# Kernel optimization log

Hardware: AMD Instinct MI355X
Metric: run time of the kernel (lower is better)

The kernel has to match this reference:

```python
import jax, jax.numpy as jnp
import numpy as np

N_NODES = 100000
N_EDGES = 1600000
N_CLASS = 26
HIDDEN = 128


def gcn_conv(x, W, b, row, col, ew, n):
    """PyG GCNConv with normalize=True, add_self_loops=True (fill 1.0).

    row/col/ew already include self-loops. x: [N, Fin], W: [Fin, Fout].
    """
    deg = jax.ops.segment_sum(ew, col, num_segments=n)            # [N]
    dis = jnp.where(deg > 0, jax.lax.rsqrt(jnp.maximum(deg, 1e-30)), 0.0)
    norm = dis[row] * ew * dis[col]                               # [E+N]
    h = x @ W                                                     # [N, Fout]
    msg = h[row] * norm[:, None]                                  # gather + scale
    out = jax.ops.segment_sum(msg, col, num_segments=n)           # scatter-add
    return out + b


def setup_inputs() -> dict:
    key = jax.random.key(0)
    k1, k2, k3, k4, k5, k6, k7, k8, k9 = jax.random.split(key, 9)
    x = jax.random.normal(k1, (N_NODES, N_CLASS), dtype=jnp.float32)
    edge_index = jax.random.randint(k2, (2, N_EDGES), 0, N_NODES, dtype=jnp.int64)
    edge_weight = jax.random.uniform(k3, (N_EDGES,), dtype=jnp.float32)
    s1 = 1.0 / np.sqrt(N_CLASS)
    s2 = 1.0 / np.sqrt(HIDDEN)
    W1 = jax.random.uniform(k4, (N_CLASS, HIDDEN), jnp.float32, -s1, s1)
    b1 = jnp.zeros((HIDDEN,), jnp.float32)
    W2 = jax.random.uniform(k5, (HIDDEN, HIDDEN), jnp.float32, -s2, s2)
    b2 = jnp.zeros((HIDDEN,), jnp.float32)
    Wfc = jax.random.uniform(k6, (HIDDEN, N_CLASS), jnp.float32, -s2, s2)
    bfc = jax.random.uniform(k7, (N_CLASS,), jnp.float32, -s2, s2)
    return {"x": x, "edge_index": edge_index, "edge_weight": edge_weight,
            "W1": W1, "b1": b1, "W2": W2, "b2": b2, "Wfc": Wfc, "bfc": bfc}


def reference(x, edge_index, edge_weight, W1, b1, W2, b2, Wfc, bfc):
    n = x.shape[0]
    loop = jnp.arange(n, dtype=edge_index.dtype)
    row = jnp.concatenate([edge_index[0], loop])   # sources (with self-loops)
    col = jnp.concatenate([edge_index[1], loop])   # targets
    ew = jnp.concatenate([edge_weight, jnp.ones((n,), edge_weight.dtype)])
    h = jax.nn.relu(gcn_conv(x, W1, b1, row, col, ew, n))
    h = jax.nn.relu(gcn_conv(h, W2, b2, row, col, ew, n))
    return h @ Wfc + bfc
```

## Files before the change

kernel.cpp:

```cpp
#include <hip/hip_runtime.h>
#include <hip/hip_fp16.h>

#define N_NODES 100000
#define N_EDGES 1600000
#define HIDDEN  128
#define N_CLASS 26

#define BUK_SHIFT 8
#define BUK_DSTS  256
#define NBUK      391
#define BUK_CAP   5120
#define PB_EDGES  4096
#define PB_BLOCKS ((N_EDGES + PB_EDGES - 1) / PB_EDGES)

typedef _Float16 f16x2 __attribute__((ext_vector_type(2)));

__device__ __forceinline__ float fdot2(__half2 a, __half2 b, float c) {
#if __has_builtin(__builtin_amdgcn_fdot2)
    union { __half2 h; f16x2 v; } ua, ub;
    ua.h = a; ub.h = b;
    return __builtin_amdgcn_fdot2(ua.v, ub.v, c, false);
#else
    float2 fa = __half22float2(a), fb = __half22float2(b);
    return c + fa.x * fb.x + fa.y * fb.y;
#endif
}

union U4 { uint4 u; __half2 h[4]; };
union U2 { uint2 u; __half2 h[2]; };
union UW { int i; __half2 h; };


__global__ __launch_bounds__(512) void bucket_kernel(const int* __restrict__ row,
                                                     const int* __restrict__ col,
                                                     const float* __restrict__ ew,
                                                     int* __restrict__ bukcnt,
                                                     int2* __restrict__ stage) {
    __shared__ int2 outst[PB_EDGES];
    __shared__ unsigned short bukof[PB_EDGES];
    __shared__ int cnt[NBUK], ofs[NBUK], cur[NBUK], gt[NBUK];
    __shared__ int sc[512];
    const int tid = threadIdx.x;
    const int e0 = blockIdx.x * PB_EDGES;
    const int nvalid = min(PB_EDGES, N_EDGES - e0);

    for (int b = tid; b < NBUK; b += 512) { cnt[b] = 0; cur[b] = 0; }
    __syncthreads();

    int mykey[8]; float myw[8]; int mybuk[8];
#pragma unroll
    for (int i = 0; i < 8; ++i) {
        int idx = tid + i * 512;
        mybuk[i] = -1;
        if (idx < nvalid) {
            int e = e0 + idx;
            int d = col[e], r = row[e];
            int buk = d >> BUK_SHIFT;
            mykey[i] = ((d & (BUK_DSTS - 1)) << 17) | r;
            myw[i] = ew[e];
            mybuk[i] = buk;
            atomicAdd(&cnt[buk], 1);
        }
    }
    __syncthreads();

    {
        int c = (tid < NBUK) ? cnt[tid] : 0;
        sc[tid] = c;
        __syncthreads();
        for (int o = 1; o < 512; o <<= 1) {
            int v = (tid >= o) ? sc[tid - o] : 0;
            __syncthreads();
            sc[tid] += v;
            __syncthreads();
        }
        if (tid < NBUK) ofs[tid] = sc[tid] - c;
        __syncthreads();
    }

#pragma unroll
    for (int i = 0; i < 8; ++i) {
        if (mybuk[i] >= 0) {
            int s = ofs[mybuk[i]] + atomicAdd(&cur[mybuk[i]], 1);
            outst[s] = make_int2(mykey[i], __float_as_int(myw[i]));
            bukof[s] = (unsigned short)mybuk[i];
        }
    }
    __syncthreads();

    if (tid < NBUK) {
        int c = cnt[tid];
        int gb = (c > 0) ? atomicAdd(&bukcnt[tid], c) : 0;
        gt[tid] = tid * BUK_CAP + gb;
    }
    __syncthreads();

    for (int i = tid; i < nvalid; i += 512) {
        int b = bukof[i];
        stage[(size_t)gt[b] + (i - ofs[b])] = outst[i];
    }
}


__global__ void bukscan_kernel(const int* __restrict__ bukcnt, int* __restrict__ bukbase,
                               int* __restrict__ start) {
    __shared__ int s[512];
    int tid = threadIdx.x;
    int c = (tid < NBUK) ? bukcnt[tid] : 0;
    s[tid] = c;
    __syncthreads();
    for (int o = 1; o < 512; o <<= 1) {
        int v = (tid >= o) ? s[tid - o] : 0;
        __syncthreads();
        s[tid] += v;
        __syncthreads();
    }
    if (tid < NBUK) bukbase[tid] = s[tid] - c;
    if (tid == 0) start[N_NODES] = N_EDGES;
}


__global__ __launch_bounds__(1024) void csr_kernel(const int2* __restrict__ stage,
                                                   const int* __restrict__ bukcnt,
                                                   const int* __restrict__ bukbase,
                                                   const float* __restrict__ x,
                                                   int* __restrict__ start,
                                                   float* __restrict__ dinv,
                                                   __half* __restrict__ x16,
                                                   int2* __restrict__ packed,
                                                   int* __restrict__ perm) {
    __shared__ unsigned int cnt5[BUK_DSTS];
    __shared__ int ofs5[BUK_DSTS];
    __shared__ unsigned int cur5[BUK_DSTS];
    __shared__ float deg5[BUK_DSTS];
    __shared__ float dv5[BUK_DSTS];
    __shared__ int sc[BUK_DSTS];
    __shared__ int dhist[128];
    __shared__ int dcur[128];
    const int tid = threadIdx.x;
    const int b = blockIdx.x;
    const int total = bukcnt[b];
    const int base = bukbase[b];
    const int2* st = stage + (size_t)b * BUK_CAP;

    if (tid < BUK_DSTS) { cnt5[tid] = 0; cur5[tid] = 0; deg5[tid] = 0.0f; }
    if (tid < 128) { dhist[tid] = 0; dcur[tid] = 0; }
    __syncthreads();

    for (int i = tid; i < total; i += 1024) {
        int2 en = st[i];
        int dl = en.x >> 17;
        atomicAdd(&cnt5[dl], 1u);
        atomicAdd(&deg5[dl], __int_as_float(en.y));
    }
    __syncthreads();

    {
        int c = (tid < BUK_DSTS) ? (int)cnt5[tid] : 0;
        if (tid < BUK_DSTS) sc[tid] = c;
        __syncthreads();
        for (int o = 1; o < BUK_DSTS; o <<= 1) {
            int v = 0;
            if (tid < BUK_DSTS && tid >= o) v = sc[tid - o];
            __syncthreads();
            if (tid < BUK_DSTS) sc[tid] += v;
            __syncthreads();
        }
        if (tid < BUK_DSTS) ofs5[tid] = sc[tid] - c;
        __syncthreads();
    }

    int myd = -1;
    {
        int d = (b << BUK_SHIFT) + tid;
        if (tid < BUK_DSTS && d < N_NODES) {
            myd = min((int)cnt5[tid], 127);
            atomicAdd(&dhist[myd], 1);
        }
    }

    if (tid < BUK_DSTS) {
        int d = (b << BUK_SHIFT) + tid;
        if (d < N_NODES) {
            float dv = rsqrtf(deg5[tid] + 1.0f);
            dv5[tid] = dv;
            dinv[d] = dv;
            start[d] = base + ofs5[tid];
        }
    }
    __syncthreads();

    if (tid < 128) sc[tid] = dhist[tid];
    __syncthreads();
    for (int o = 1; o < 128; o <<= 1) {
        int v = 0;
        if (tid < 128 && tid >= o) v = sc[tid - o];
        __syncthreads();
        if (tid < 128) sc[tid] += v;
        __syncthreads();
    }
    if (myd >= 0) {
        int rank = sc[myd] - dhist[myd] + atomicAdd(&dcur[myd], 1);
        perm[(b << BUK_SHIFT) + rank] = (b << BUK_SHIFT) + tid;
    }

    for (int t = tid; t < BUK_DSTS * 32; t += 1024) {
        int j = t >> 5, l = t & 31;
        int d = (b << BUK_SHIFT) + j;
        if (d < N_NODES) {
            float v = (l < N_CLASS) ? x[(size_t)d * N_CLASS + l] * dv5[j] : 0.0f;
            x16[((size_t)d << 5) + l] = __float2half(v);
        }
    }

    for (int i = tid; i < total; i += 1024) {
        int2 en = st[i];
        int dl = en.x >> 17;
        int src = en.x & 0x1FFFF;
        unsigned int r = atomicAdd(&cur5[dl], 1u);
        unsigned int hw = __half_as_ushort(__float2half(__int_as_float(en.y)));
        packed[(size_t)base + ofs5[dl] + (int)r] = make_int2(src, (int)(hw | (hw << 16)));
    }
}


__global__ __launch_bounds__(256) void layer1_kernel(const __half* __restrict__ x16,
                                                     const int* __restrict__ start,
                                                     const int2* __restrict__ packed,
                                                     const float* __restrict__ dinv,
                                                     const int* __restrict__ perm,
                                                     const float* __restrict__ W1,
                                                     const float* __restrict__ b1,
                                                     __half* __restrict__ h16) {
    __shared__ float axs[32][32];
    __shared__ int gl[32];
    const int tid = threadIdx.x;
    const int nb = blockIdx.x * 32;
    {
        const int j = tid >> 3;
        const int l = tid & 7;
        const int g = perm[nb + j];
        if (l == 0) gl[j] = g;
        const uint2* X = reinterpret_cast<const uint2*>(x16);
        U2 sv; sv.u = X[((size_t)g << 3) + l];
        __half2 acc0 = sv.h[0], acc1 = sv.h[1];
        int s = start[g], t = start[g + 1];
        int i = s;
        for (; i + 8 <= t; i += 8) {
            int2 pk[8]; U2 vv[8];
#pragma unroll
            for (int u = 0; u < 8; ++u) pk[u] = packed[i + u];
#pragma unroll
            for (int u = 0; u < 8; ++u) vv[u].u = X[((size_t)pk[u].x << 3) + l];
#pragma unroll
            for (int u = 0; u < 8; ++u) {
                UW w; w.i = pk[u].y;
                acc0 = __hfma2(w.h, vv[u].h[0], acc0);
                acc1 = __hfma2(w.h, vv[u].h[1], acc1);
            }
        }
        for (; i < t; ++i) {
            int2 p = packed[i];
            U2 v; v.u = X[((size_t)p.x << 3) + l];
            UW w; w.i = p.y;
            acc0 = __hfma2(w.h, v.h[0], acc0); acc1 = __hfma2(w.h, v.h[1], acc1);
        }
        float dg = dinv[g];
        float2 a = __half22float2(acc0), bb = __half22float2(acc1);
        *reinterpret_cast<float4*>(&axs[j][l * 4]) =
            make_float4(dg * a.x, dg * a.y, dg * bb.x, dg * bb.y);
    }
    __syncthreads();
    const int c = tid & 127;
    const int half = tid >> 7;
    float w[N_CLASS];
#pragma unroll
    for (int k = 0; k < N_CLASS; ++k) w[k] = W1[k * HIDDEN + c];
    const float bias = b1[c];
#pragma unroll
    for (int tt = 0; tt < 16; ++tt) {
        int n = half + 2 * tt;
        float acc = bias;
#pragma unroll
        for (int k = 0; k < N_CLASS; ++k) acc += axs[n][k] * w[k];
        h16[(size_t)gl[n] * HIDDEN + c] = __float2half(fmaxf(acc, 0.0f));
    }
}


#define CB_NODES 128
__global__ __launch_bounds__(512) void gemmC_kernel(const __half* __restrict__ h16,
                                                    const float* __restrict__ W2,
                                                    const float* __restrict__ dinv,
                                                    __half* __restrict__ p16) {
    __shared__ __half2 hs2[CB_NODES][HIDDEN / 2];
    __shared__ __half2 ws2[HIDDEN / 2][HIDDEN];
    const int tid = threadIdx.x;
    const int nb = blockIdx.x * CB_NODES;
    for (int t = tid; t < HIDDEN / 2 * HIDDEN; t += 512) {
        int k2 = t >> 7, c = t & 127;
        ws2[k2][c] = __floats2half2_rn(W2[(2 * k2) * HIDDEN + c], W2[(2 * k2 + 1) * HIDDEN + c]);
    }
    for (int t = tid; t < CB_NODES * 16; t += 512) {
        int node = nb + (t >> 4);
        reinterpret_cast<uint4*>(hs2)[t] =
            (node < N_NODES)
                ? reinterpret_cast<const uint4*>(h16)[(size_t)node * 16 + (t & 15)]
                : make_uint4(0u, 0u, 0u, 0u);
    }
    __syncthreads();
    const int c4 = (tid & 31) * 4;
    const int n0 = (tid >> 5) * 8;
    float acc[8][4] = {};
    for (int k2 = 0; k2 < HIDDEN / 2; k2 += 2) {
        U4 wa, wb;
        wa.u = *reinterpret_cast<const uint4*>(&ws2[k2][c4]);
        wb.u = *reinterpret_cast<const uint4*>(&ws2[k2 + 1][c4]);
#pragma unroll
        for (int i = 0; i < 8; ++i) {
            U2 hv; hv.u = *reinterpret_cast<const uint2*>(&hs2[n0 + i][k2]);
#pragma unroll
            for (int q = 0; q < 4; ++q) {
                acc[i][q] = fdot2(hv.h[0], wa.h[q], acc[i][q]);
                acc[i][q] = fdot2(hv.h[1], wb.h[q], acc[i][q]);
            }
        }
    }
#pragma unroll
    for (int i = 0; i < 8; ++i) {
        int node = nb + n0 + i;
        if (node < N_NODES) {
            float d = dinv[node];
            union { __half2 h2[2]; uint2 u; } pk;
            pk.h2[0] = __floats2half2_rn(d * acc[i][0], d * acc[i][1]);
            pk.h2[1] = __floats2half2_rn(d * acc[i][2], d * acc[i][3]);
            *reinterpret_cast<uint2*>(&p16[(size_t)node * HIDDEN + c4]) = pk.u;
        }
    }
}


__global__ __launch_bounds__(256) void aggfc_kernel(const __half* __restrict__ p16,
                                                    const int* __restrict__ start,
                                                    const int2* __restrict__ packed,
                                                    const float* __restrict__ dinv,
                                                    const int* __restrict__ perm,
                                                    const float* __restrict__ b2,
                                                    const float* __restrict__ Wfc,
                                                    const float* __restrict__ bfc,
                                                    float* __restrict__ out) {
    __shared__ __half2 wf2[HIDDEN / 2][N_CLASS];
    __shared__ float bfs[N_CLASS];
    __shared__ __half2 zs2[16][65];
    const int tid = threadIdx.x;
    for (int t = tid; t < HIDDEN / 2 * N_CLASS; t += 256) {
        int k2 = t / N_CLASS, j = t % N_CLASS;
        wf2[k2][j] = __floats2half2_rn(Wfc[(2 * k2) * N_CLASS + j], Wfc[(2 * k2 + 1) * N_CLASS + j]);
    }
    if (tid < N_CLASS) bfs[tid] = bfc[tid];
    __syncthreads();

    const int grp = tid >> 4;
    const int l   = tid & 15;
    const int g   = perm[blockIdx.x * 16 + grp];
    const uint4* P = reinterpret_cast<const uint4*>(p16);

    U4 sv; sv.u = P[((size_t)g << 4) + l];
    __half2 acc0 = sv.h[0], acc1 = sv.h[1], acc2 = sv.h[2], acc3 = sv.h[3];

    int s = start[g], t = start[g + 1];
    int i = s;
    for (; i + 8 <= t; i += 8) {
        int2 pk[8]; U4 vv[8];
#pragma unroll
        for (int u = 0; u < 8; ++u) pk[u] = packed[i + u];
#pragma unroll
        for (int u = 0; u < 8; ++u) vv[u].u = P[((size_t)pk[u].x << 4) + l];
#pragma unroll
        for (int u = 0; u < 8; ++u) {
            UW w; w.i = pk[u].y;
            acc0 = __hfma2(w.h, vv[u].h[0], acc0);
            acc1 = __hfma2(w.h, vv[u].h[1], acc1);
            acc2 = __hfma2(w.h, vv[u].h[2], acc2);
            acc3 = __hfma2(w.h, vv[u].h[3], acc3);
        }
    }
    for (; i + 4 <= t; i += 4) {
        int2 pk[4]; U4 vv[4];
#pragma unroll
        for (int u = 0; u < 4; ++u) pk[u] = packed[i + u];
#pragma unroll
        for (int u = 0; u < 4; ++u) vv[u].u = P[((size_t)pk[u].x << 4) + l];
#pragma unroll
        for (int u = 0; u < 4; ++u) {
            UW w; w.i = pk[u].y;
            acc0 = __hfma2(w.h, vv[u].h[0], acc0);
            acc1 = __hfma2(w.h, vv[u].h[1], acc1);
            acc2 = __hfma2(w.h, vv[u].h[2], acc2);
            acc3 = __hfma2(w.h, vv[u].h[3], acc3);
        }
    }
    for (; i < t; ++i) {
        int2 p = packed[i];
        U4 v; v.u = P[((size_t)p.x << 4) + l];
        UW w; w.i = p.y;
        acc0 = __hfma2(w.h, v.h[0], acc0); acc1 = __hfma2(w.h, v.h[1], acc1);
        acc2 = __hfma2(w.h, v.h[2], acc2); acc3 = __hfma2(w.h, v.h[3], acc3);
    }

    const float dg = dinv[g];
    const int f = l * 8;
    float4 ba = *reinterpret_cast<const float4*>(&b2[f]);
    float4 bb = *reinterpret_cast<const float4*>(&b2[f + 4]);
    float2 f0 = __half22float2(acc0), f1 = __half22float2(acc1);
    float2 f2 = __half22float2(acc2), f3 = __half22float2(acc3);
    zs2[grp][l * 4 + 0] = __floats2half2_rn(fmaxf(dg * f0.x + ba.x, 0.f), fmaxf(dg * f0.y + ba.y, 0.f));
    zs2[grp][l * 4 + 1] = __floats2half2_rn(fmaxf(dg * f1.x + ba.z, 0.f), fmaxf(dg * f1.y + ba.w, 0.f));
    zs2[grp][l * 4 + 2] = __floats2half2_rn(fmaxf(dg * f2.x + bb.x, 0.f), fmaxf(dg * f2.y + bb.y, 0.f));
    zs2[grp][l * 4 + 3] = __floats2half2_rn(fmaxf(dg * f3.x + bb.z, 0.f), fmaxf(dg * f3.y + bb.w, 0.f));
#pragma unroll
    for (int jj = l; jj < N_CLASS; jj += 16) {
        float accf = bfs[jj];
#pragma unroll 16
        for (int k2 = 0; k2 < HIDDEN / 2; ++k2)
            accf = fdot2(zs2[grp][k2], wf2[k2][jj], accf);
        out[(size_t)g * N_CLASS + jj] = accf;
    }
}


extern "C" void kernel_launch(void* const* d_in, const int* in_sizes, int n_in,
                              void* d_out, int out_size, void* d_ws, size_t ws_size,
                              hipStream_t stream) {
    const float* x   = (const float*)d_in[0];
    const int*   ei  = (const int*)  d_in[1];
    const float* ew  = (const float*)d_in[2];
    const float* W1  = (const float*)d_in[3];
    const float* b1  = (const float*)d_in[4];
    const float* W2  = (const float*)d_in[5];
    const float* b2  = (const float*)d_in[6];
    const float* Wfc = (const float*)d_in[7];
    const float* bfc = (const float*)d_in[8];
    float* out = (float*)d_out;

    const int n = N_NODES, E = N_EDGES;
    const int* row = ei;
    const int* col = ei + E;

    char* ws = (char*)d_ws;
    size_t off = 0;
    auto alloc = [&](size_t bytes) -> void* {
        void* ptr = ws + off;
        off += (bytes + 255) & ~(size_t)255;
        return ptr;
    };
    int*   bukcnt  = (int*)  alloc(NBUK * 4);
    int*   bukbase = (int*)  alloc(NBUK * 4);
    float* dinv    = (float*)alloc((size_t)n * 4);
    int*   start   = (int*)  alloc((size_t)(n + 1) * 4);
    int*   perm    = (int*)  alloc((size_t)n * 4);
    int2*  packed  = (int2*) alloc((size_t)E * 8);
    __half* x16    = (__half*)alloc((size_t)n * 32 * 2);
    __half* h16    = (__half*)alloc((size_t)n * HIDDEN * 2 < (size_t)NBUK * BUK_CAP * 8
                                        ? (size_t)NBUK * BUK_CAP * 8
                                        : (size_t)n * HIDDEN * 2);
    __half* p16    = (__half*)alloc((size_t)n * HIDDEN * 2);
    int2*  stage   = (int2*)h16;

    hipMemsetAsync(bukcnt, 0, NBUK * 4, stream);
    bucket_kernel<<<PB_BLOCKS, 512, 0, stream>>>(row, col, ew, bukcnt, stage);
    bukscan_kernel<<<1, 512, 0, stream>>>(bukcnt, bukbase, start);
    csr_kernel<<<NBUK, 1024, 0, stream>>>(stage, bukcnt, bukbase, x, start, dinv, x16, packed, perm);

    layer1_kernel<<<(n + 31) / 32, 256, 0, stream>>>(x16, start, packed, dinv, perm, W1, b1, h16);

    gemmC_kernel<<<(n + CB_NODES - 1) / CB_NODES, 512, 0, stream>>>(h16, W2, dinv, p16);
    aggfc_kernel<<<(n + 15) / 16, 256, 0, stream>>>(p16, start, packed, dinv, perm, b2, Wfc, bfc, out);
}
```

Measured before the change: 224.0 us.

## Use wave-shuffle scans, register-cached edges in CSR build, drop 8-way unroll

```diff
diff --git a/kernel.cpp b/kernel.cpp
--- a/kernel.cpp
+++ b/kernel.cpp
@@ -30,6 +30,15 @@
 union U2 { uint2 u; __half2 h[2]; };
 union UW { int i; __half2 h; };
 
+__device__ __forceinline__ int wave_iscan(int v, int lane) {
+#pragma unroll
+    for (int o = 1; o < 64; o <<= 1) {
+        int u = __shfl_up(v, o, 64);
+        if (lane >= o) v += u;
+    }
+    return v;
+}
+
 
 __global__ __launch_bounds__(512) void bucket_kernel(const int* __restrict__ row,
                                                      const int* __restrict__ col,
@@ -39,8 +48,10 @@
     __shared__ int2 outst[PB_EDGES];
     __shared__ unsigned short bukof[PB_EDGES];
     __shared__ int cnt[NBUK], ofs[NBUK], cur[NBUK], gt[NBUK];
-    __shared__ int sc[512];
-    const int tid = threadIdx.x;
+    __shared__ int wsum[8], woff[8];
+    const int tid = threadIdx.x;
+    const int lane = tid & 63;
+    const int wid = tid >> 6;
     const int e0 = blockIdx.x * PB_EDGES;
     const int nvalid = min(PB_EDGES, N_EDGES - e0);
 
@@ -66,15 +77,16 @@
 
     {
         int c = (tid < NBUK) ? cnt[tid] : 0;
-        sc[tid] = c;
-        __syncthreads();
-        for (int o = 1; o < 512; o <<= 1) {
-            int v = (tid >= o) ? sc[tid - o] : 0;
-            __syncthreads();
-            sc[tid] += v;
-            __syncthreads();
-        }
-        if (tid < NBUK) ofs[tid] = sc[tid] - c;
+        int sv = wave_iscan(c, lane);
+        if (lane == 63) wsum[wid] = sv;
+        __syncthreads();
+        if (tid < 8) {
+            int acc = 0;
+            for (int k = 0; k < tid; ++k) acc += wsum[k];
+            woff[tid] = acc;
+        }
+        __syncthreads();
+        if (tid < NBUK) ofs[tid] = sv - c + woff[wid];
         __syncthreads();
     }
 
@@ -102,42 +114,47 @@
 }
 
 
-__global__ void bukscan_kernel(const int* __restrict__ bukcnt, int* __restrict__ bukbase,
-                               int* __restrict__ start) {
-    __shared__ int s[512];
-    int tid = threadIdx.x;
+__global__ __launch_bounds__(512) void bukscan_kernel(const int* __restrict__ bukcnt,
+                                                      int* __restrict__ bukbase,
+                                                      int* __restrict__ start) {
+    __shared__ int wsum[8], woff[8];
+    const int tid = threadIdx.x;
+    const int lane = tid & 63;
+    const int wid = tid >> 6;
     int c = (tid < NBUK) ? bukcnt[tid] : 0;
-    s[tid] = c;
-    __syncthreads();
-    for (int o = 1; o < 512; o <<= 1) {
-        int v = (tid >= o) ? s[tid - o] : 0;
-        __syncthreads();
-        s[tid] += v;
-        __syncthreads();
-    }
-    if (tid < NBUK) bukbase[tid] = s[tid] - c;
+    int sv = wave_iscan(c, lane);
+    if (lane == 63) wsum[wid] = sv;
+    __syncthreads();
+    if (tid < 8) {
+        int acc = 0;
+        for (int k = 0; k < tid; ++k) acc += wsum[k];
+        woff[tid] = acc;
+    }
+    __syncthreads();
+    if (tid < NBUK) bukbase[tid] = sv - c + woff[wid];
     if (tid == 0) start[N_NODES] = N_EDGES;
 }
 
 
-__global__ __launch_bounds__(1024) void csr_kernel(const int2* __restrict__ stage,
-                                                   const int* __restrict__ bukcnt,
-                                                   const int* __restrict__ bukbase,
-                                                   const float* __restrict__ x,
-                                                   int* __restrict__ start,
-                                                   float* __restrict__ dinv,
-                                                   __half* __restrict__ x16,
-                                                   int2* __restrict__ packed,
-                                                   int* __restrict__ perm) {
+__global__ __launch_bounds__(512) void csr_kernel(const int2* __restrict__ stage,
+                                                  const int* __restrict__ bukcnt,
+                                                  const int* __restrict__ bukbase,
+                                                  const float* __restrict__ x,
+                                                  int* __restrict__ start,
+                                                  float* __restrict__ dinv,
+                                                  __half* __restrict__ x16,
+                                                  int2* __restrict__ packed,
+                                                  int* __restrict__ perm) {
     __shared__ unsigned int cnt5[BUK_DSTS];
     __shared__ int ofs5[BUK_DSTS];
     __shared__ unsigned int cur5[BUK_DSTS];
     __shared__ float deg5[BUK_DSTS];
     __shared__ float dv5[BUK_DSTS];
-    __shared__ int sc[BUK_DSTS];
-    __shared__ int dhist[128];
-    __shared__ int dcur[128];
-    const int tid = threadIdx.x;
+    __shared__ int dhist[128], dcur[128], hofs[128];
+    __shared__ int wsum[8], woff[8];
+    const int tid = threadIdx.x;
+    const int lane = tid & 63;
+    const int wid = tid >> 6;
     const int b = blockIdx.x;
     const int total = bukcnt[b];
     const int base = bukbase[b];
@@ -147,41 +164,41 @@
     if (tid < 128) { dhist[tid] = 0; dcur[tid] = 0; }
     __syncthreads();
 
-    for (int i = tid; i < total; i += 1024) {
-        int2 en = st[i];
-        int dl = en.x >> 17;
-        atomicAdd(&cnt5[dl], 1u);
-        atomicAdd(&deg5[dl], __int_as_float(en.y));
+    int2 en[10];
+    int nmine = 0;
+#pragma unroll
+    for (int k = 0; k < 10; ++k) {
+        int idx = tid + k * 512;
+        if (idx < total) {
+            en[k] = st[idx];
+            int dl = en[k].x >> 17;
+            atomicAdd(&cnt5[dl], 1u);
+            atomicAdd(&deg5[dl], __int_as_float(en[k].y));
+            nmine = k + 1;
+        }
     }
     __syncthreads();
 
     {
         int c = (tid < BUK_DSTS) ? (int)cnt5[tid] : 0;
-        if (tid < BUK_DSTS) sc[tid] = c;
-        __syncthreads();
-        for (int o = 1; o < BUK_DSTS; o <<= 1) {
-            int v = 0;
-            if (tid < BUK_DSTS && tid >= o) v = sc[tid - o];
-            __syncthreads();
-            if (tid < BUK_DSTS) sc[tid] += v;
-            __syncthreads();
-        }
-        if (tid < BUK_DSTS) ofs5[tid] = sc[tid] - c;
-        __syncthreads();
+        int sv = wave_iscan(c, lane);
+        if (lane == 63 && wid < 4) wsum[wid] = sv;
+        __syncthreads();
+        if (tid < 4) {
+            int acc = 0;
+            for (int k = 0; k < tid; ++k) acc += wsum[k];
+            woff[tid] = acc;
+        }
+        __syncthreads();
+        if (tid < BUK_DSTS) ofs5[tid] = sv - c + woff[wid];
     }
 
     int myd = -1;
-    {
-        int d = (b << BUK_SHIFT) + tid;
-        if (tid < BUK_DSTS && d < N_NODES) {
-            myd = min((int)cnt5[tid], 127);
-            atomicAdd(&dhist[myd], 1);
-        }
-    }
-
     if (tid < BUK_DSTS) {
         int d = (b << BUK_SHIFT) + tid;
         if (d < N_NODES) {
+            myd = min((int)cnt5[tid], 127);
+            atomicAdd(&dhist[myd], 1);
             float dv = rsqrtf(deg5[tid] + 1.0f);
             dv5[tid] = dv;
             dinv[d] = dv;
@@ -190,36 +207,40 @@
     }
     __syncthreads();
 
-    if (tid < 128) sc[tid] = dhist[tid];
-    __syncthreads();
-    for (int o = 1; o < 128; o <<= 1) {
-        int v = 0;
-        if (tid < 128 && tid >= o) v = sc[tid - o];
-        __syncthreads();
-        if (tid < 128) sc[tid] += v;
+    {
+        int c = (tid < 128) ? dhist[tid] : 0;
+        int sv = wave_iscan(c, lane);
+        if (lane == 63 && wid < 2) wsum[wid] = sv;
+        __syncthreads();
+        if (tid < 128) hofs[tid] = sv - c + ((wid == 1) ? wsum[0] : 0);
         __syncthreads();
     }
     if (myd >= 0) {
-        int rank = sc[myd] - dhist[myd] + atomicAdd(&dcur[myd], 1);
+        int rank = hofs[myd] + atomicAdd(&dcur[myd], 1);
         perm[(b << BUK_SHIFT) + rank] = (b << BUK_SHIFT) + tid;
     }
 
-    for (int t = tid; t < BUK_DSTS * 32; t += 1024) {
-        int j = t >> 5, l = t & 31;
+    for (int t = tid; t < BUK_DSTS * 16; t += 512) {
+        int j = t >> 4, p = t & 15;
         int d = (b << BUK_SHIFT) + j;
         if (d < N_NODES) {
-            float v = (l < N_CLASS) ? x[(size_t)d * N_CLASS + l] * dv5[j] : 0.0f;
-            x16[((size_t)d << 5) + l] = __float2half(v);
-        }
-    }
-
-    for (int i = tid; i < total; i += 1024) {
-        int2 en = st[i];
-        int dl = en.x >> 17;
-        int src = en.x & 0x1FFFF;
-        unsigned int r = atomicAdd(&cur5[dl], 1u);
-        unsigned int hw = __half_as_ushort(__float2half(__int_as_float(en.y)));
-        packed[(size_t)base + ofs5[dl] + (int)r] = make_int2(src, (int)(hw | (hw << 16)));
+            int l0 = 2 * p, l1 = 2 * p + 1;
+            float dv = dv5[j];
+            float v0 = (l0 < N_CLASS) ? x[(size_t)d * N_CLASS + l0] * dv : 0.0f;
+            float v1 = (l1 < N_CLASS) ? x[(size_t)d * N_CLASS + l1] * dv : 0.0f;
+            reinterpret_cast<__half2*>(x16)[((size_t)d << 4) + p] = __floats2half2_rn(v0, v1);
+        }
+    }
+
+#pragma unroll
+    for (int k = 0; k < 10; ++k) {
+        if (k < nmine) {
+            int dl = en[k].x >> 17;
+            int src = en[k].x & 0x1FFFF;
+            unsigned int r = atomicAdd(&cur5[dl], 1u);
+            unsigned int hw = __half_as_ushort(__float2half(__int_as_float(en[k].y)));
+            packed[(size_t)base + ofs5[dl] + (int)r] = make_int2(src, (int)(hw | (hw << 16)));
+        }
     }
 }
 
@@ -370,35 +391,22 @@
 
     int s = start[g], t = start[g + 1];
     int i = s;
-    for (; i + 8 <= t; i += 8) {
-        int2 pk[8]; U4 vv[8];
-#pragma unroll
-        for (int u = 0; u < 8; ++u) pk[u] = packed[i + u];
-#pragma unroll
-        for (int u = 0; u < 8; ++u) vv[u].u = P[((size_t)pk[u].x << 4) + l];
-#pragma unroll
-        for (int u = 0; u < 8; ++u) {
-            UW w; w.i = pk[u].y;
-            acc0 = __hfma2(w.h, vv[u].h[0], acc0);
-            acc1 = __hfma2(w.h, vv[u].h[1], acc1);
-            acc2 = __hfma2(w.h, vv[u].h[2], acc2);
-            acc3 = __hfma2(w.h, vv[u].h[3], acc3);
-        }
-    }
     for (; i + 4 <= t; i += 4) {
-        int2 pk[4]; U4 vv[4];
-#pragma unroll
-        for (int u = 0; u < 4; ++u) pk[u] = packed[i + u];
-#pragma unroll
-        for (int u = 0; u < 4; ++u) vv[u].u = P[((size_t)pk[u].x << 4) + l];
-#pragma unroll
-        for (int u = 0; u < 4; ++u) {
-            UW w; w.i = pk[u].y;
-            acc0 = __hfma2(w.h, vv[u].h[0], acc0);
-            acc1 = __hfma2(w.h, vv[u].h[1], acc1);
-            acc2 = __hfma2(w.h, vv[u].h[2], acc2);
-            acc3 = __hfma2(w.h, vv[u].h[3], acc3);
-        }
+        int2 pa = packed[i], pb = packed[i + 1], pc = packed[i + 2], pd = packed[i + 3];
+        U4 va, vb, vc, vd;
+        va.u = P[((size_t)pa.x << 4) + l];
+        vb.u = P[((size_t)pb.x << 4) + l];
+        vc.u = P[((size_t)pc.x << 4) + l];
+        vd.u = P[((size_t)pd.x << 4) + l];
+        UW wa, wb, wc, wd; wa.i = pa.y; wb.i = pb.y; wc.i = pc.y; wd.i = pd.y;
+        acc0 = __hfma2(wa.h, va.h[0], acc0); acc1 = __hfma2(wa.h, va.h[1], acc1);
+        acc2 = __hfma2(wa.h, va.h[2], acc2); acc3 = __hfma2(wa.h, va.h[3], acc3);
+        acc0 = __hfma2(wb.h, vb.h[0], acc0); acc1 = __hfma2(wb.h, vb.h[1], acc1);
+        acc2 = __hfma2(wb.h, vb.h[2], acc2); acc3 = __hfma2(wb.h, vb.h[3], acc3);
+        acc0 = __hfma2(wc.h, vc.h[0], acc0); acc1 = __hfma2(wc.h, vc.h[1], acc1);
+        acc2 = __hfma2(wc.h, vc.h[2], acc2); acc3 = __hfma2(wc.h, vc.h[3], acc3);
+        acc0 = __hfma2(wd.h, vd.h[0], acc0); acc1 = __hfma2(wd.h, vd.h[1], acc1);
+        acc2 = __hfma2(wd.h, vd.h[2], acc2); acc3 = __hfma2(wd.h, vd.h[3], acc3);
     }
     for (; i < t; ++i) {
         int2 p = packed[i];
@@ -470,7 +478,7 @@
     hipMemsetAsync(bukcnt, 0, NBUK * 4, stream);
     bucket_kernel<<<PB_BLOCKS, 512, 0, stream>>>(row, col, ew, bukcnt, stage);
     bukscan_kernel<<<1, 512, 0, stream>>>(bukcnt, bukbase, start);
-    csr_kernel<<<NBUK, 1024, 0, stream>>>(stage, bukcnt, bukbase, x, start, dinv, x16, packed, perm);
+    csr_kernel<<<NBUK, 512, 0, stream>>>(stage, bukcnt, bukbase, x, start, dinv, x16, packed, perm);
 
     layer1_kernel<<<(n + 31) / 32, 256, 0, stream>>>(x16, start, packed, dinv, perm, W1, b1, h16);
 
```

Result: faster. 219.3 us (median of 2 runs) (-2.1%).
